# Kernel optimization log

Measured on AMD Instinct MI355X. Metric: run time of the kernel, lower is better.

The kernel has to match this reference:

```python
import jax, jax.numpy as jnp
import numpy as np

EPS = 1e-8
N, E, T, HH, HE, HD = 20000, 320000, 4, 64, 16, 128


def _merge(a):
    # 'm d t -> (m t) d'
    m, d, t = a.shape
    return a.transpose(0, 2, 1).reshape(m * t, d)


def _sep(a, t):
    # '(m t) d -> m d t'
    mt, d = a.shape
    return a.reshape(mt // t, t, d).transpose(0, 2, 1)


def _mlp2(x, w1, b1, w2, b2, last_act):
    y = jax.nn.silu(x @ w1 + b1)
    y = y @ w2 + b2
    return jax.nn.silu(y) if last_act else y


def setup_inputs() -> dict:
    key = jax.random.key(0)
    ks = jax.random.split(key, 16)

    def lin(k, i, o):
        return jax.random.normal(k, (i, o), jnp.float32) / np.sqrt(i)

    in_edge = HH * 2 + 1 + HE  # 145
    return {
        "x": jax.random.normal(ks[0], (N, 3, T), jnp.float32),
        "h": jax.random.normal(ks[1], (N, HH, T), jnp.float32),
        "edge_index": jax.random.randint(ks[2], (2, E), 0, N),
        "edge_attr": jax.random.normal(ks[3], (E, HE, T), jnp.float32),
        "batch": jnp.zeros((N,), jnp.int64),
        "edge_w1": lin(ks[4], in_edge, HD), "edge_b1": jnp.zeros((HD,), jnp.float32),
        "edge_w2": lin(ks[5], HD, HD), "edge_b2": jnp.zeros((HD,), jnp.float32),
        "coord_w1": lin(ks[6], HD, HD), "coord_b1": jnp.zeros((HD,), jnp.float32),
        "coord_w2": lin(ks[7], HD, 1), "coord_b2": jnp.zeros((1,), jnp.float32),
        "node_w1": lin(ks[8], HH + HD, HD), "node_b1": jnp.zeros((HD,), jnp.float32),
        "node_w2": lin(ks[9], HD, HH), "node_b2": jnp.zeros((HH,), jnp.float32),
    }


def reference(x, h, edge_index, edge_attr, batch,
              edge_w1, edge_b1, edge_w2, edge_b2,
              coord_w1, coord_b1, coord_w2, coord_b2,
              node_w1, node_b1, node_w2, node_b2):
    row, col = edge_index[0], edge_index[1]
    t = x.shape[-1]
    n = x.shape[0]

    x_ij = x[row] - x[col]                                  # [E,3,T]
    x_ij_norm2 = (x_ij ** 2).sum(axis=1, keepdims=True)     # [E,1,T]

    m_in = jnp.concatenate((h[row], h[col], x_ij_norm2, edge_attr), axis=1)  # [E,2Hh+1+He,T]
    m_ij = _mlp2(_merge(m_in), edge_w1, edge_b1, edge_w2, edge_b2, True)     # [ET,HD]

    m_i = jax.ops.segment_sum(_sep(m_ij, t), row, num_segments=n)           # [N,HD,T]

    h_cat = jnp.concatenate((_merge(h), _merge(m_i)), axis=-1)               # [NT,Hh+HD]
    h_new = _sep(_mlp2(h_cat, node_w1, node_b1, node_w2, node_b2, False), t) # [N,Hh,T]

    coord_m_ij = _mlp2(m_ij, coord_w1, coord_b1, coord_w2, coord_b2, False)  # [ET,1]
    coord_m_ij = coord_m_ij / (jnp.sqrt(_merge(x_ij_norm2) + EPS) + 1.0)

    agg = jax.ops.segment_sum(_sep(coord_m_ij, t) * x_ij, row, num_segments=n)  # [N,3,T]
    cnt = jax.ops.segment_sum(jnp.ones((row.shape[0],), x.dtype), row, num_segments=n)
    x_new = x + agg / jnp.maximum(cnt, 1.0)[:, None, None]
    return (x_new, h_new)
```

## Files before the change

kernel.cpp:

```cpp
#include <hip/hip_runtime.h>
#include <hip/hip_bf16.h>
#include <math.h>

#define T 4
#define HH 64
#define HE 16
#define HD 128
#define EPSF 1e-8f

#define TE 16
#define ROWS 64
#define LDA 168
#define TN 16
#define LDAN 200

using frag8 = __attribute__((ext_vector_type(8))) short;
using f32x4 = __attribute__((ext_vector_type(4))) float;

__device__ __forceinline__ float silu_f(float v) {
    return v * __builtin_amdgcn_rcpf(1.f + __expf(-v));
}

__device__ __forceinline__ unsigned short f2b(float f) {
    __hip_bfloat16 h = __float2bfloat16(f);
    union { __hip_bfloat16 h; unsigned short u; } v; v.h = h;
    return v.u;
}
__device__ __forceinline__ unsigned pk2(float a, float b) {
    __hip_bfloat162 h2 = __float22bfloat162_rn(make_float2(a, b));
    union { __hip_bfloat162 h; unsigned u; } v; v.h = h2;
    return v.u;
}
__device__ __forceinline__ float b2f(unsigned u16) {
    union { unsigned u; float f; } v; v.u = u16 << 16; return v.f;
}
__device__ __forceinline__ void lds_fence() {
    asm volatile("s_waitcnt lgkmcnt(0)" ::: "memory");
}

__global__ void prep_fused(const float* __restrict__ w1, const float* __restrict__ w2,
                           const float* __restrict__ cw1, const float* __restrict__ nw1,
                           const float* __restrict__ nw2, unsigned short* __restrict__ wb,
                           const float* __restrict__ h, unsigned short* __restrict__ hb,
                           const int* __restrict__ ei, int* __restrict__ deg,
                           int NB_H, int N, int E)
{
    int b = blockIdx.x;
    if (b < 336) {
        int i = b * 256 + threadIdx.x;
        if (i < 20480) {
            int n = i / 160, k = i - n * 160;
            float v;
            if (k < 128)      v = w1[k * 128 + n];
            else if (k < 144) v = w1[(129 + (k - 128)) * 128 + n];
            else if (k == 144) v = w1[128 * 128 + n];
            else              v = 0.f;
            wb[i] = f2b(v);
        } else if (i < 36864) {
            int j = i - 20480; int n = j >> 7, k = j & 127;
            wb[i] = f2b(w2[k * 128 + n]);
        } else if (i < 53248) {
            int j = i - 36864; int n = j >> 7, k = j & 127;
            wb[i] = f2b(cw1[k * 128 + n]);
        } else if (i < 77824) {
            int j = i - 53248; int n = j / 192, k = j - n * 192;
            wb[i] = f2b(nw1[k * 128 + n]);
        } else if (i < 86016) {
            int j = i - 77824; int n = j >> 7, k = j & 127;
            wb[i] = f2b(nw2[k * 64 + n]);
        }
    } else if (b < 336 + NB_H) {
        int i = (b - 336) * 256 + threadIdx.x;
        if (i < N * 64) {
            float4 v = *(const float4*)(h + (size_t)i * 4);
            int n = i >> 6, d = i & 63;
            size_t base = (size_t)n * 256 + d;
            hb[base + 0]   = f2b(v.x);
            hb[base + 64]  = f2b(v.y);
            hb[base + 128] = f2b(v.z);
            hb[base + 192] = f2b(v.w);
        }
    } else {
        int e = (b - 336 - NB_H) * 256 + threadIdx.x;
        if (e < E) atomicAdd(&deg[ei[e]], 1);
    }
}

__global__ __launch_bounds__(1024)
void scan_kernel(const int* __restrict__ deg, int* __restrict__ start, int N) {
    __shared__ int part[1024];
    int tid = threadIdx.x;
    int chunk = (N + 1023) >> 10;
    int b0 = tid * chunk;
    int s = 0;
    for (int i = 0; i < chunk; ++i) { int idx = b0 + i; if (idx < N) s += deg[idx]; }
    part[tid] = s;
    __syncthreads();
    for (int off = 1; off < 1024; off <<= 1) {
        int v = (tid >= off) ? part[tid - off] : 0;
        __syncthreads();
        part[tid] += v;
        __syncthreads();
    }
    int prefix = (tid > 0) ? part[tid - 1] : 0;
    for (int i = 0; i < chunk; ++i) {
        int idx = b0 + i;
        if (idx < N) { start[idx] = prefix; prefix += deg[idx]; }
    }
    if (tid == 1023) start[N] = part[1023];
}

__global__ void scatter_kernel(const int* __restrict__ ei, const int* __restrict__ start,
                               int* __restrict__ cursor, int* __restrict__ list, int E) {
    int e = blockIdx.x * 256 + threadIdx.x;
    if (e < E) {
        int r = ei[e];
        int p = atomicAdd(&cursor[r], 1);
        list[start[r] + p] = e;
    }
}

__global__ __launch_bounds__(256, 7)
void edge_kernel(const float* __restrict__ x, const unsigned short* __restrict__ hb,
                 const int* __restrict__ ei, const float* __restrict__ ea,
                 const int* __restrict__ list,
                 const unsigned short* __restrict__ w1b,
                 const unsigned short* __restrict__ w2b,
                 const unsigned short* __restrict__ cw1b,
                 const float* __restrict__ b1, const float* __restrict__ b2,
                 const float* __restrict__ cb1, const float* __restrict__ cb2,
                 const float* __restrict__ cw2,
                 float* __restrict__ m_i,
                 float* __restrict__ agg,
                 int N, int E)
{
    __shared__ unsigned short sA[ROWS * LDA];
    __shared__ float sXij[TE * 12];
    __shared__ float sNorm[ROWS];
    __shared__ int   sNode[TE];
    __shared__ int   sPN[2];
    __shared__ float sCoord[ROWS];

    const int tid  = threadIdx.x;
    const int e0   = blockIdx.x * TE;
    const int lane = tid & 63;
    const int wid  = tid >> 6;
    const int eb   = wid * 4;

    if (tid < ROWS) sCoord[tid] = 0.f;
    if (tid == 0) {
        sPN[0] = (e0 > 0)      ? ei[list[e0 - 1]]  : -2;
        sPN[1] = (e0 + TE < E) ? ei[list[e0 + TE]] : -2;
    }

    int node8 = 0;
    {
        int le = lane >> 1, half = lane & 1;
        int p = e0 + eb + le;
        if (lane < 8 && p < E) {
            int eid = list[p];
            node8 = ei[half ? (E + eid) : eid];
            if (half == 0) sNode[eb + le] = node8;
        }
    }
    if (lane < 48) {
        int le = lane / 12, i = lane - le * 12;
        int p = e0 + eb + le;
        float d = 0.f;
        if (p < E) {
            int eid = list[p];
            d = x[ei[eid] * 12 + i] - x[ei[E + eid] * 12 + i];
        }
        sXij[(eb + le) * 12 + i] = d;
    }
    {
        int half = lane >> 5, t = (lane >> 3) & 3, chunk = lane & 7;
        #pragma unroll
        for (int le = 0; le < 4; ++le) {
            int p = e0 + eb + le;
            if (p < E) {
                int nid = __shfl(node8, le * 2 + half);
                uint4 v = *((const uint4*)hb + (size_t)nid * 32 + t * 8 + chunk);
                *(uint4*)&sA[((eb + le) * 4 + t) * LDA + half * 64 + chunk * 8] = v;
            }
        }
    }
    if (lane < 16) {
        int le = lane >> 2, eh0 = (lane & 3) * 4;
        int p = e0 + eb + le;
        if (p < E) {
            const float4* ap = (const float4*)(ea + (size_t)list[p] * 64);
            float4 av[4];
            #pragma unroll
            for (int q = 0; q < 4; ++q) av[q] = ap[eh0 + q];
            #pragma unroll
            for (int t = 0; t < 4; ++t) {
                uint2 u;
                u.x = pk2(((const float*)&av[0])[t], ((const float*)&av[1])[t]);
                u.y = pk2(((const float*)&av[2])[t], ((const float*)&av[3])[t]);
                *(uint2*)&sA[((eb + le) * 4 + t) * LDA + 128 + eh0] = u;
            }
        }
    }
    lds_fence();
    if (lane < 16) {
        int row = wid * 16 + lane;
        int le = eb + (lane >> 2), t = lane & 3;
        float a0 = sXij[le * 12 + t], a1 = sXij[le * 12 + 4 + t], a2 = sXij[le * 12 + 8 + t];
        float n2 = a0 * a0 + a1 * a1 + a2 * a2;
        sNorm[row] = n2;
        uint4 z = {0, 0, 0, 0};
        *(uint4*)&sA[row * LDA + 144] = z;
        *(uint4*)&sA[row * LDA + 152] = z;
        sA[row * LDA + 144] = f2b(n2);
    }
    __syncthreads();

    const int lrow = lane & 15;
    const int quad = lane >> 4;
    const int c0 = wid * 2;

    f32x4 acc[4][2];
    {
        float bv0 = b1[c0 * 16 + lrow], bv1 = b1[(c0 + 1) * 16 + lrow];
        #pragma unroll
        for (int m = 0; m < 4; ++m) {
            acc[m][0] = (f32x4){bv0, bv0, bv0, bv0};
            acc[m][1] = (f32x4){bv1, bv1, bv1, bv1};
        }
    }
    __builtin_amdgcn_s_setprio(1);
    #pragma unroll
    for (int kb = 0; kb < 5; ++kb) {
        frag8 a[4], b[2];
        #pragma unroll
        for (int m = 0; m < 4; ++m)
            a[m] = *(const frag8*)&sA[(m * 16 + lrow) * LDA + kb * 32 + quad * 8];
        #pragma unroll
        for (int n = 0; n < 2; ++n)
            b[n] = *(const frag8*)&w1b[((c0 + n) * 16 + lrow) * 160 + kb * 32 + quad * 8];
        #pragma unroll
        for (int m = 0; m < 4; ++m)
            #pragma unroll
            for (int n = 0; n < 2; ++n)
                acc[m][n] = __builtin_amdgcn_mfma_f32_16x16x32_bf16(a[m], b[n], acc[m][n], 0, 0, 0);
    }
    __builtin_amdgcn_s_setprio(0);
    __syncthreads();

    #pragma unroll
    for (int n = 0; n < 2; ++n) {
        int col = (c0 + n) * 16 + lrow;
        #pragma unroll
        for (int m = 0; m < 4; ++m)
            #pragma unroll
            for (int r = 0; r < 4; ++r)
                sA[(m * 16 + quad * 4 + r) * LDA + col] = f2b(silu_f(acc[m][n][r]));
    }
    __syncthreads();

    {
        float bv0 = b2[c0 * 16 + lrow], bv1 = b2[(c0 + 1) * 16 + lrow];
        #pragma unroll
        for (int m = 0; m < 4; ++m) {
            acc[m][0] = (f32x4){bv0, bv0, bv0, bv0};
            acc[m][1] = (f32x4){bv1, bv1, bv1, bv1};
        }
    }
    __builtin_amdgcn_s_setprio(1);
    #pragma unroll
    for (int kb = 0; kb < 4; ++kb) {
        frag8 a[4], b[2];
        #pragma unroll
        for (int m = 0; m < 4; ++m)
            a[m] = *(const frag8*)&sA[(m * 16 + lrow) * LDA + kb * 32 + quad * 8];
        #pragma unroll
        for (int n = 0; n < 2; ++n)
            b[n] = *(const frag8*)&w2b[((c0 + n) * 16 + lrow) * 128 + kb * 32 + quad * 8];
        #pragma unroll
        for (int m = 0; m < 4; ++m)
            #pragma unroll
            for (int n = 0; n < 2; ++n)
                acc[m][n] = __builtin_amdgcn_mfma_f32_16x16x32_bf16(a[m], b[n], acc[m][n], 0, 0, 0);
    }
    __builtin_amdgcn_s_setprio(0);
    __syncthreads();

    #pragma unroll
    for (int n = 0; n < 2; ++n) {
        int col = (c0 + n) * 16 + lrow;
        #pragma unroll
        for (int m = 0; m < 4; ++m)
            #pragma unroll
            for (int r = 0; r < 4; ++r)
                sA[(m * 16 + quad * 4 + r) * LDA + col] = f2b(silu_f(acc[m][n][r]));
    }
    __syncthreads();

    {
        float bv0 = cb1[c0 * 16 + lrow], bv1 = cb1[(c0 + 1) * 16 + lrow];
        #pragma unroll
        for (int m = 0; m < 4; ++m) {
            acc[m][0] = (f32x4){bv0, bv0, bv0, bv0};
            acc[m][1] = (f32x4){bv1, bv1, bv1, bv1};
        }
    }
    __builtin_amdgcn_s_setprio(1);
    #pragma unroll
    for (int kb = 0; kb < 4; ++kb) {
        frag8 a[4], b[2];
        #pragma unroll
        for (int m = 0; m < 4; ++m)
            a[m] = *(const frag8*)&sA[(m * 16 + lrow) * LDA + kb * 32 + quad * 8];
        #pragma unroll
        for (int n = 0; n < 2; ++n)
            b[n] = *(const frag8*)&cw1b[((c0 + n) * 16 + lrow) * 128 + kb * 32 + quad * 8];
        #pragma unroll
        for (int m = 0; m < 4; ++m)
            #pragma unroll
            for (int n = 0; n < 2; ++n)
                acc[m][n] = __builtin_amdgcn_mfma_f32_16x16x32_bf16(a[m], b[n], acc[m][n], 0, 0, 0);
    }
    __builtin_amdgcn_s_setprio(0);
    {
        float v[16];
        #pragma unroll
        for (int j = 0; j < 16; ++j) v[j] = 0.f;
        #pragma unroll
        for (int n = 0; n < 2; ++n) {
            int col = (c0 + n) * 16 + lrow;
            float cw2v = cw2[col];
            #pragma unroll
            for (int m = 0; m < 4; ++m)
                #pragma unroll
                for (int r = 0; r < 4; ++r)
                    v[m * 4 + r] += silu_f(acc[m][n][r]) * cw2v;
        }
        #pragma unroll
        for (int s = 8; s >= 1; s >>= 1) {
            #pragma unroll
            for (int j = 0; j < s; ++j) {
                float sel = (lrow & s) ? v[j] : v[j + s];
                float oth = __shfl_xor(sel, s);
                v[j] = ((lrow & s) ? v[j + s] : v[j]) + oth;
            }
        }
        atomicAdd(&sCoord[(lrow >> 2) * 16 + quad * 4 + (lrow & 3)], v[0]);
    }

    {
        const int t = tid & 3, c = tid >> 2;
        const int prevN = sPN[0], nextN = sPN[1];
        float r0 = 0.f, r1 = 0.f;
        int cur = sNode[0];
        int ls = 0;
        #pragma unroll
        for (int le = 0; le < TE; ++le) {
            int nd = sNode[le];
            if (nd != cur) {
                if (cur >= 0) {
                    float* d0 = &m_i[(size_t)cur * 512 + tid];
                    if (ls == 0 && prevN == cur) { atomicAdd(d0, r0); atomicAdd(d0 + 256, r1); }
                    else                         { d0[0] = r0; d0[256] = r1; }
                }
                r0 = 0.f; r1 = 0.f; cur = nd; ls = le;
            }
            if (nd >= 0) {
                r0 += b2f((unsigned)sA[(le * 4 + t) * LDA + c]);
                r1 += b2f((unsigned)sA[(le * 4 + t) * LDA + c + 64]);
            }
        }
        if (cur >= 0) {
            float* d0 = &m_i[(size_t)cur * 512 + tid];
            if ((ls == 0 && prevN == cur) || nextN == cur) { atomicAdd(d0, r0); atomicAdd(d0 + 256, r1); }
            else                                           { d0[0] = r0; d0[256] = r1; }
        }
    }
    __syncthreads();

    if (tid < ROWS) {
        float c = (sCoord[tid] + cb2[0]) *
                  __builtin_amdgcn_rcpf(__builtin_amdgcn_sqrtf(sNorm[tid] + EPSF) + 1.f);
        sCoord[tid] = c;
    }
    lds_fence();

    if (tid < 12) {
        int t = tid & 3;
        float run = 0.f;
        int cur = sNode[0];
        for (int le = 0; le < TE; ++le) {
            int nd = sNode[le];
            if (nd != cur) {
                if (cur >= 0) atomicAdd(&agg[(size_t)cur * 12 + tid], run);
                run = 0.f; cur = nd;
            }
            if (nd >= 0) run += sCoord[le * 4 + t] * sXij[le * 12 + tid];
        }
        if (cur >= 0) atomicAdd(&agg[(size_t)cur * 12 + tid], run);
    }
}

__global__ __launch_bounds__(256, 6)
void node_kernel(const unsigned short* __restrict__ hb, const float* __restrict__ m_i,
                 const unsigned short* __restrict__ nw1b,
                 const unsigned short* __restrict__ nw2b,
                 const float* __restrict__ nb1, const float* __restrict__ nb2,
                 const float* __restrict__ x, const float* __restrict__ agg,
                 const int* __restrict__ deg,
                 float* __restrict__ out_x, float* __restrict__ out_h, int N)
{
    __shared__ unsigned short sA[64 * LDAN];

    const int tid = threadIdx.x;
    const int n0  = blockIdx.x * TN;

    if (tid < 192) {
        int g = n0 * 12 + tid;
        if (g < N * 12) {
            int n = n0 + tid / 12;
            out_x[g] = x[g] + agg[g] * __builtin_amdgcn_rcpf(fmaxf((float)deg[n], 1.f));
        }
    }

    #pragma unroll
    for (int z = 0; z < 2; ++z) {
        int c = z * 256 + tid;
        int ln = c >> 5, t = (c >> 3) & 3, chunk = c & 7;
        int node = n0 + ln;
        if (node < N) {
            uint4 v = *((const uint4*)hb + (size_t)node * 32 + t * 8 + chunk);
            *(uint4*)&sA[(ln * 4 + t) * LDAN + chunk * 8] = v;
        }
    }
    for (int c = tid; c < 512; c += 256) {
        int ln = c >> 5, hd0 = (c & 31) * 4;
        int node = n0 + ln;
        if (node < N) {
            const float4* mp = (const float4*)(m_i + (size_t)node * 512);
            float4 mv[4];
            #pragma unroll
            for (int q = 0; q < 4; ++q) mv[q] = mp[hd0 + q];
            #pragma unroll
            for (int t = 0; t < 4; ++t) {
                uint2 u;
                u.x = pk2(((const float*)&mv[0])[t], ((const float*)&mv[1])[t]);
                u.y = pk2(((const float*)&mv[2])[t], ((const float*)&mv[3])[t]);
                *(uint2*)&sA[(ln * 4 + t) * LDAN + 64 + hd0] = u;
            }
        }
    }
    __syncthreads();

    const int lane = tid & 63;
    const int wid  = tid >> 6;
    const int lrow = lane & 15;
    const int quad = lane >> 4;
    const int c0 = wid * 2;

    f32x4 acc[4][2];
    {
        float bv0 = nb1[c0 * 16 + lrow], bv1 = nb1[(c0 + 1) * 16 + lrow];
        #pragma unroll
        for (int m = 0; m < 4; ++m) {
            acc[m][0] = (f32x4){bv0, bv0, bv0, bv0};
            acc[m][1] = (f32x4){bv1, bv1, bv1, bv1};
        }
    }
    __builtin_amdgcn_s_setprio(1);
    #pragma unroll
    for (int kb = 0; kb < 6; ++kb) {
        frag8 a[4], b[2];
        #pragma unroll
        for (int m = 0; m < 4; ++m)
            a[m] = *(const frag8*)&sA[(m * 16 + lrow) * LDAN + kb * 32 + quad * 8];
        #pragma unroll
        for (int n = 0; n < 2; ++n)
            b[n] = *(const frag8*)&nw1b[((c0 + n) * 16 + lrow) * 192 + kb * 32 + quad * 8];
        #pragma unroll
        for (int m = 0; m < 4; ++m)
            #pragma unroll
            for (int n = 0; n < 2; ++n)
                acc[m][n] = __builtin_amdgcn_mfma_f32_16x16x32_bf16(a[m], b[n], acc[m][n], 0, 0, 0);
    }
    __builtin_amdgcn_s_setprio(0);
    __syncthreads();

    #pragma unroll
    for (int n = 0; n < 2; ++n) {
        int col = (c0 + n) * 16 + lrow;
        #pragma unroll
        for (int m = 0; m < 4; ++m)
            #pragma unroll
            for (int r = 0; r < 4; ++r)
                sA[(m * 16 + quad * 4 + r) * LDAN + col] = f2b(silu_f(acc[m][n][r]));
    }
    __syncthreads();

    f32x4 acc2[4];
    {
        float bv = nb2[wid * 16 + lrow];
        #pragma unroll
        for (int m = 0; m < 4; ++m) acc2[m] = (f32x4){bv, bv, bv, bv};
    }
    __builtin_amdgcn_s_setprio(1);
    #pragma unroll
    for (int kb = 0; kb < 4; ++kb) {
        frag8 a[4];
        #pragma unroll
        for (int m = 0; m < 4; ++m)
            a[m] = *(const frag8*)&sA[(m * 16 + lrow) * LDAN + kb * 32 + quad * 8];
        frag8 b = *(const frag8*)&nw2b[(wid * 16 + lrow) * 128 + kb * 32 + quad * 8];
        #pragma unroll
        for (int m = 0; m < 4; ++m)
            acc2[m] = __builtin_amdgcn_mfma_f32_16x16x32_bf16(a[m], b, acc2[m], 0, 0, 0);
    }
    __builtin_amdgcn_s_setprio(0);
    #pragma unroll
    for (int m = 0; m < 4; ++m) {
        int node = n0 + m * 4 + quad;
        if (node < N) {
            float* op = out_h + (size_t)node * 256 + (wid * 16 + lrow) * 4;
            float4 ov = { acc2[m][0], acc2[m][1], acc2[m][2], acc2[m][3] };
            *(float4*)op = ov;
        }
    }
}

extern "C" void kernel_launch(void* const* d_in, const int* in_sizes, int n_in,
                              void* d_out, int out_size, void* d_ws, size_t ws_size,
                              hipStream_t stream)
{
    const float* x   = (const float*)d_in[0];
    const float* h   = (const float*)d_in[1];
    const int*   ei  = (const int*)d_in[2];
    const float* ea  = (const float*)d_in[3];
    const float* w1  = (const float*)d_in[5];
    const float* b1  = (const float*)d_in[6];
    const float* w2  = (const float*)d_in[7];
    const float* b2  = (const float*)d_in[8];
    const float* cw1 = (const float*)d_in[9];
    const float* cb1 = (const float*)d_in[10];
    const float* cw2 = (const float*)d_in[11];
    const float* cb2 = (const float*)d_in[12];
    const float* nw1 = (const float*)d_in[13];
    const float* nb1 = (const float*)d_in[14];
    const float* nw2 = (const float*)d_in[15];
    const float* nb2 = (const float*)d_in[16];

    const int N = in_sizes[0] / 12;
    const int E = in_sizes[2] / 2;

    char* ws = (char*)d_ws;
    unsigned short* wb = (unsigned short*)ws;
    size_t o = 172032;
    int*   deg    = (int*)(ws + o);    o += (size_t)N * 4;
    int*   cursor = (int*)(ws + o);    o += (size_t)N * 4;
    float* agg    = (float*)(ws + o);  o += (size_t)N * 48;
    size_t zero_end = o;
    int*   start  = (int*)(ws + o);    o += (size_t)(N + 1) * 4;
    o = (o + 1023) & ~(size_t)1023;
    int*   list   = (int*)(ws + o);    o += (size_t)E * 4;
    o = (o + 1023) & ~(size_t)1023;
    unsigned short* hb = (unsigned short*)(ws + o); o += (size_t)N * 512;
    o = (o + 1023) & ~(size_t)1023;
    float* m_i    = (float*)(ws + o);

    const unsigned short* w1b  = wb;
    const unsigned short* w2b  = wb + 20480;
    const unsigned short* cw1b = wb + 36864;
    const unsigned short* nw1b = wb + 53248;
    const unsigned short* nw2b = wb + 77824;

    const int NB_H = (N * 64 + 255) / 256;
    const int NB_E = (E + 255) / 256;

    hipMemsetAsync(deg, 0, zero_end - 172032, stream);
    hipMemsetAsync(m_i, 0, (size_t)N * 512 * sizeof(float), stream);
    prep_fused<<<336 + NB_H + NB_E, 256, 0, stream>>>(
        w1, w2, cw1, nw1, nw2, wb, h, hb, ei, deg, NB_H, N, E);
    scan_kernel<<<1, 1024, 0, stream>>>(deg, start, N);
    scatter_kernel<<<NB_E, 256, 0, stream>>>(ei, start, cursor, list, E);

    float* out_x = (float*)d_out;
    float* out_h = out_x + (size_t)N * 12;

    edge_kernel<<<(E + TE - 1) / TE, 256, 0, stream>>>(
        x, hb, ei, ea, list, w1b, w2b, cw1b, b1, b2, cb1, cb2, cw2, m_i, agg, N, E);
    node_kernel<<<(N + TN - 1) / TN, 256, 0, stream>>>(
        hb, m_i, nw1b, nw2b, nb1, nb2, x, agg, deg, out_x, out_h, N);
}
```

Baseline: 555.3 us.

## Fold m_i zeroing into prep kernel and trim LDS traffic in edge kernel

Drops the separate memset of the m_i buffer and zeroes it with extra blocks inside the prep kernel, saving one launch. In the edge kernel the squared edge-length is now computed from register shuffles instead of a fenced LDS read-back. The segment reduction reads bf16 pairs as 32-bit words. In the node kernel the out_x update moves after the loads are issued. These are several small unrelated tweaks, and the extra blocks make the prep grid larger.

```diff
diff --git a/kernel.cpp b/kernel.cpp
--- a/kernel.cpp
+++ b/kernel.cpp
@@ -43,7 +43,8 @@
                            const float* __restrict__ nw2, unsigned short* __restrict__ wb,
                            const float* __restrict__ h, unsigned short* __restrict__ hb,
                            const int* __restrict__ ei, int* __restrict__ deg,
-                           int NB_H, int N, int E)
+                           float* __restrict__ m_i,
+                           int NB_H, int NB_E, int N, int E)
 {
     int b = blockIdx.x;
     if (b < 336) {
@@ -80,9 +81,15 @@
             hb[base + 128] = f2b(v.z);
             hb[base + 192] = f2b(v.w);
         }
-    } else {
+    } else if (b < 336 + NB_H + NB_E) {
         int e = (b - 336 - NB_H) * 256 + threadIdx.x;
         if (e < E) atomicAdd(&deg[ei[e]], 1);
+    } else {
+        int i = (b - 336 - NB_H - NB_E) * 256 + threadIdx.x;
+        if (i < N * 128) {
+            float4 z = {0.f, 0.f, 0.f, 0.f};
+            ((float4*)m_i)[i] = z;
+        }
     }
 }
 
@@ -163,15 +170,15 @@
             if (half == 0) sNode[eb + le] = node8;
         }
     }
+    float xd = 0.f;
     if (lane < 48) {
         int le = lane / 12, i = lane - le * 12;
         int p = e0 + eb + le;
-        float d = 0.f;
         if (p < E) {
             int eid = list[p];
-            d = x[ei[eid] * 12 + i] - x[ei[E + eid] * 12 + i];
-        }
-        sXij[(eb + le) * 12 + i] = d;
+            xd = x[ei[eid] * 12 + i] - x[ei[E + eid] * 12 + i];
+        }
+        sXij[(eb + le) * 12 + i] = xd;
     }
     {
         int half = lane >> 5, t = (lane >> 3) & 3, chunk = lane & 7;
@@ -202,17 +209,20 @@
             }
         }
     }
-    lds_fence();
-    if (lane < 16) {
-        int row = wid * 16 + lane;
-        int le = eb + (lane >> 2), t = lane & 3;
-        float a0 = sXij[le * 12 + t], a1 = sXij[le * 12 + 4 + t], a2 = sXij[le * 12 + 8 + t];
-        float n2 = a0 * a0 + a1 * a1 + a2 * a2;
-        sNorm[row] = n2;
-        uint4 z = {0, 0, 0, 0};
-        *(uint4*)&sA[row * LDA + 144] = z;
-        *(uint4*)&sA[row * LDA + 152] = z;
-        sA[row * LDA + 144] = f2b(n2);
+    {
+        int sb = (lane >> 2) * 12 + (lane & 3);
+        float a0 = __shfl(xd, sb);
+        float a1 = __shfl(xd, sb + 4);
+        float a2 = __shfl(xd, sb + 8);
+        if (lane < 16) {
+            int row = wid * 16 + lane;
+            float n2 = a0 * a0 + a1 * a1 + a2 * a2;
+            sNorm[row] = n2;
+            uint4 z = {0, 0, 0, 0};
+            *(uint4*)&sA[row * LDA + 144] = z;
+            *(uint4*)&sA[row * LDA + 152] = z;
+            sA[row * LDA + 144] = f2b(n2);
+        }
     }
     __syncthreads();
 
@@ -350,6 +360,8 @@
 
     {
         const int t = tid & 3, c = tid >> 2;
+        const int cw = c >> 1;
+        const unsigned shl = (c & 1) ? 0u : 16u;
         const int prevN = sPN[0], nextN = sPN[1];
         float r0 = 0.f, r1 = 0.f;
         int cur = sNode[0];
@@ -366,8 +378,13 @@
                 r0 = 0.f; r1 = 0.f; cur = nd; ls = le;
             }
             if (nd >= 0) {
-                r0 += b2f((unsigned)sA[(le * 4 + t) * LDA + c]);
-                r1 += b2f((unsigned)sA[(le * 4 + t) * LDA + c + 64]);
+                const unsigned* rp = (const unsigned*)&sA[(le * 4 + t) * LDA];
+                unsigned u0 = rp[cw];
+                unsigned u1 = rp[cw + 32];
+                union { unsigned u; float f; } f0, f1;
+                f0.u = (u0 << shl) & 0xffff0000u;
+                f1.u = (u1 << shl) & 0xffff0000u;
+                r0 += f0.f; r1 += f1.f;
             }
         }
         if (cur >= 0) {
@@ -415,14 +432,6 @@
     const int tid = threadIdx.x;
     const int n0  = blockIdx.x * TN;
 
-    if (tid < 192) {
-        int g = n0 * 12 + tid;
-        if (g < N * 12) {
-            int n = n0 + tid / 12;
-            out_x[g] = x[g] + agg[g] * __builtin_amdgcn_rcpf(fmaxf((float)deg[n], 1.f));
-        }
-    }
-
     #pragma unroll
     for (int z = 0; z < 2; ++z) {
         int c = z * 256 + tid;
@@ -448,6 +457,13 @@
                 u.y = pk2(((const float*)&mv[2])[t], ((const float*)&mv[3])[t]);
                 *(uint2*)&sA[(ln * 4 + t) * LDAN + 64 + hd0] = u;
             }
+        }
+    }
+    if (tid < 192) {
+        int g = n0 * 12 + tid;
+        if (g < N * 12) {
+            int n = n0 + tid / 12;
+            out_x[g] = x[g] + agg[g] * __builtin_amdgcn_rcpf(fmaxf((float)deg[n], 1.f));
         }
     }
     __syncthreads();
@@ -574,11 +590,11 @@
 
     const int NB_H = (N * 64 + 255) / 256;
     const int NB_E = (E + 255) / 256;
+    const int NB_M = (N * 128 + 255) / 256;
 
     hipMemsetAsync(deg, 0, zero_end - 172032, stream);
-    hipMemsetAsync(m_i, 0, (size_t)N * 512 * sizeof(float), stream);
-    prep_fused<<<336 + NB_H + NB_E, 256, 0, stream>>>(
-        w1, w2, cw1, nw1, nw2, wb, h, hb, ei, deg, NB_H, N, E);
+    prep_fused<<<336 + NB_H + NB_E + NB_M, 256, 0, stream>>>(
+        w1, w2, cw1, nw1, nw2, wb, h, hb, ei, deg, m_i, NB_H, NB_E, N, E);
     scan_kernel<<<1, 1024, 0, stream>>>(deg, start, N);
     scatter_kernel<<<NB_E, 256, 0, stream>>>(ei, start, cursor, list, E);
 
```

Result: no change. 557.2 us (+0.4%).
